# Optimization experiments

Hardware: AMD Instinct MI355X
Metric: run time of the kernel (lower is better)

## Reference

```python
import jax, jax.numpy as jnp
import numpy as np

DPITCH_RANGE = 24.0
SCALE = 1.0

B, T, ND, SD, H = 8192, 256, 8, 3, 64
HIST = 64
L = T - HIST  # generated LSTM steps; L+1 outputs emitted
IN = ND + SD + 1


def setup_inputs() -> dict:
    key = jax.random.key(0)
    ks = jax.random.split(key, 11)
    s = 1.0 / np.sqrt(H)

    def u(k, shape):
        return jax.random.uniform(k, shape, jnp.float32, -s, s)

    return {
        "noise": jax.random.normal(ks[0], (B, T, ND), jnp.float32),
        "hist_x": jax.random.normal(ks[1], (B, HIST, SD), jnp.float32) * 0.1,
        "gap_duration": jax.random.uniform(ks[2], (B, L + 1, SD - 1), jnp.float32),
        "W_ih": u(ks[3], (4 * H, IN)),
        "W_hh": u(ks[4], (4 * H, H)),
        "b_ih": u(ks[5], (4 * H,)),
        "b_hh": u(ks[6], (4 * H,)),
        "W1": u(ks[7], (H, H)),
        "b1": u(ks[8], (H,)),
        "W2": u(ks[9], (1, H)),
        "b2": u(ks[10], (1,)),
    }


def reference(noise, hist_x, gap_duration, W_ih, W_hh, b_ih, b_hh, W1, b1, W2, b2):
    hist_len = hist_x.shape[1]
    bias = b_ih + b_hh

    def lstm_cell(x, h, c):
        # PyTorch gate order: i, f, g, o
        gates = x @ W_ih.T + h @ W_hh.T + bias
        i, f, g, o = jnp.split(gates, 4, axis=-1)
        c = jax.nn.sigmoid(f) * c + jax.nn.sigmoid(i) * jnp.tanh(g)
        h = jax.nn.sigmoid(o) * jnp.tanh(c)
        return h, c

    # ---- conditioning on history ----
    dist = jnp.cumsum(hist_x[:, :, -1:], axis=1)                 # [B,HIST,1]
    cond_in = jnp.concatenate([hist_x, dist, noise[:, :hist_len]], axis=-1)  # [B,HIST,IN]
    h0 = jnp.zeros((noise.shape[0], W_hh.shape[1]), noise.dtype)
    c0 = jnp.zeros_like(h0)

    def cond_step(carry, x_t):
        h, c = carry
        h, c = lstm_cell(x_t, h, c)
        return (h, c), None

    (h, c), _ = jax.lax.scan(cond_step, (h0, c0), jnp.swapaxes(cond_in, 0, 1))
    output = h                      # last LSTM output [B,H]
    dist = dist[:, -1, :]           # [B,1]

    gen_noise = noise[:, hist_len:]                               # [B,L,ND]
    # pad one zero step: the final LSTM update is computed but unused
    gen_noise = jnp.concatenate(
        [gen_noise, jnp.zeros((gen_noise.shape[0], 1, gen_noise.shape[2]), gen_noise.dtype)], axis=1)
    xs = (jnp.swapaxes(gap_duration, 0, 1), jnp.swapaxes(gen_noise, 0, 1))

    def gen_step(carry, x_t):
        h, c, out, dist = carry
        gd, nz = x_t
        z = jnp.tanh(jnp.tanh(out @ W1.T + b1) @ W2.T + b2)       # output_net
        dp = z * DPITCH_RANGE * SCALE                             # [B,1]
        x = jnp.concatenate([gd, dp], axis=-1)                    # [B,SD]
        dist = dist + dp
        inp = jnp.concatenate([x, dist, nz], axis=-1)             # [B,IN]
        h, c = lstm_cell(inp, h, c)
        return (h, c, h, dist), x

    _, gen_xs = jax.lax.scan(gen_step, (h, c, output, dist), xs)  # [L+1,B,SD]
    output_seq = jnp.swapaxes(gen_xs, 0, 1)                       # [B,L+1,SD]
    return jnp.concatenate([hist_x, output_seq], axis=1)          # [B,HIST+L+1,SD]
```

## Files before the change

### kernel.cpp

```cpp
#include <hip/hip_runtime.h>
#include <stdint.h>

typedef unsigned short u16;
typedef unsigned int u32;
typedef __attribute__((ext_vector_type(8))) short short8v;
typedef __attribute__((ext_vector_type(4))) float f32x4;

#define NB 16
#define HISTN 64
#define TGEN 193

#define S_NOISE 2048
#define S_HIST  192
#define S_GAP   386
#define S_OUT   771

#define HROW 104

__device__ __forceinline__ float b2f(u16 u) { return __uint_as_float(((u32)u) << 16); }
__device__ __forceinline__ u16 f2b(float f) {
    u32 u = __float_as_uint(f);
    u32 r = (u + 0x7fffu + ((u >> 16) & 1u)) >> 16;
    return (u16)r;
}
__device__ __forceinline__ float rcp_(float x) { return __builtin_amdgcn_rcpf(x); }
__device__ __forceinline__ float sigf(float x) { return rcp_(1.0f + __expf(-x)); }
__device__ __forceinline__ float tanhf_(float x) {
    return __builtin_fmaf(-2.0f, rcp_(1.0f + __expf(2.0f * x)), 1.0f);
}
__device__ __forceinline__ float ldv(const void* p, int idx, bool f32) {
    return f32 ? ((const float*)p)[idx] : b2f(((const u16*)p)[idx]);
}
__device__ __forceinline__ void sync_lds() {
    asm volatile("s_waitcnt lgkmcnt(0)" ::: "memory");
    __builtin_amdgcn_s_barrier();
}

extern "C" __global__ void __launch_bounds__(512, 4)
lstm_gen_kernel(const void* __restrict__ noise, const void* __restrict__ hist_x,
                const void* __restrict__ gap, const void* __restrict__ pW_ih,
                const void* __restrict__ pW_hh, const void* __restrict__ pb_ih,
                const void* __restrict__ pb_hh, const void* __restrict__ pW1,
                const void* __restrict__ pb1, const void* __restrict__ pW2,
                const void* __restrict__ pb2, void* __restrict__ out)
{
    __shared__ u16 hst[NB * HROW];
    __shared__ float zpl[NB * 4];
    __shared__ float gds[TGEN][NB][2];
    __shared__ u16 nring[32][NB][8];
    __shared__ float dpd[NB];

    const int tid = threadIdx.x;
    const int lane = tid & 63;
    const int w = tid >> 6;
    const int lg = lane >> 4;
    const int ln = lane & 15;

    bool is_f32 = false;
    {
        const u32* p = (const u32*)pW_hh;
        for (int i = 0; i < 64; i++) {
            u32 v = p[i];
            float a = b2f((u16)(v & 0xffffu));
            float bb = b2f((u16)(v >> 16));
            if (!(fabsf(a) <= 0.5f) || !(fabsf(bb) <= 0.5f)) is_f32 = true;
        }
    }

    for (int i = tid; i < NB * HROW / 2; i += 512) ((u32*)hst)[i] = 0u;
    for (int i = tid; i < TGEN * NB * 2; i += 512) {
        int t = i >> 5, r = i & 31, b = r >> 1, k = r & 1;
        gds[t][b][k] = ldv(gap, ((size_t)blockIdx.x * NB + b) * S_GAP + t * 2 + k, is_f32);
    }

    short8v a00, a01, a02, a10, a11, a12;
#pragma unroll
    for (int T = 0; T < 2; T++) {
        const int j = (T << 5) | (w << 2) | (ln >> 2);
        const int g = ln & 3;
        const int row = (g << 6) | j;
        float wdp = ldv(pW_ih, row * 12 + 2, is_f32);
        u16 wdph = f2b(wdp);
        u16 wdpl = f2b(wdp - b2f(wdph));
        float wds = ldv(pW_ih, row * 12 + 3, is_f32);
        u16 wdsh = f2b(wds);
        u16 wdsl = f2b(wds - b2f(wdsh));
        short8v f0, f1, f2;
#pragma unroll
        for (int e = 0; e < 8; e++) {
            const int c = lg * 8 + e;
            f0[e] = (short)f2b(ldv(pW_hh, row * 64 + c, is_f32));
            f1[e] = (short)f2b(ldv(pW_hh, row * 64 + 32 + c, is_f32));
            u16 v = 0;
            if (c == 0 || c == 1) v = f2b(ldv(pW_ih, row * 12 + c, is_f32));
            else if (c == 2 || c == 3) v = wdph;
            else if (c == 4 || c == 5) v = wdsh;
            else if (c == 6) v = wdsl;
            else if (c == 7) v = wdpl;
            else if (c >= 8 && c < 16) v = f2b(ldv(pW_ih, row * 12 + (c - 4), is_f32));
            f2[e] = (short)v;
        }
        if (T == 0) { a00 = f0; a01 = f1; a02 = f2; }
        else        { a10 = f0; a11 = f1; a12 = f2; }
    }

    f32x4 bias0, bias1, wd0, wd1, ws0, ws1;
#pragma unroll
    for (int T = 0; T < 2; T++) {
        const int jc = (T << 5) | (w << 2) | lg;
        f32x4 bv, dv, sv;
#pragma unroll
        for (int q = 0; q < 4; q++) {
            const int row = (q << 6) | jc;
            bv[q] = ldv(pb_ih, row, is_f32) + ldv(pb_hh, row, is_f32);
            dv[q] = ldv(pW_ih, row * 12 + 2, is_f32);
            sv[q] = ldv(pW_ih, row * 12 + 3, is_f32);
        }
        if (T == 0) { bias0 = bv; wd0 = dv; ws0 = sv; }
        else        { bias1 = bv; wd1 = dv; ws1 = sv; }
    }

    const bool mlpw = (w >= 4);
    short8v w1F0 = {}, w1F1 = {};
    f32x4 b1v = {0.f, 0.f, 0.f, 0.f};
    float w2L[4] = {0.f, 0.f, 0.f, 0.f};
    if (mlpw) {
        const int wp = w - 4;
        const int row1 = (wp << 4) | ln;
#pragma unroll
        for (int e = 0; e < 8; e++) {
            w1F0[e] = (short)f2b(ldv(pW1, row1 * 64 + lg * 8 + e, is_f32));
            w1F1[e] = (short)f2b(ldv(pW1, row1 * 64 + 32 + lg * 8 + e, is_f32));
        }
        const int rq = (wp << 4) | (lg << 2);
#pragma unroll
        for (int q = 0; q < 4; q++) {
            b1v[q] = ldv(pb1, rq + q, is_f32);
            w2L[q] = ldv(pW2, rq + q, is_f32);
        }
    }

    const float b2v = ldv(pb2, 0, is_f32);

    const bool owner = tid < NB;
    const size_t gb = (size_t)blockIdx.x * NB + (size_t)(tid & (NB - 1));
    const u16* nz_h = (const u16*)noise + gb * S_NOISE;
    const float* nz_f = (const float*)noise + gb * S_NOISE;
    const u16* hx_h = (const u16*)hist_x + gb * S_HIST;
    const float* hx_f = (const float*)hist_x + gb * S_HIST;
    u16* out_h = (u16*)out + gb * S_OUT;
    float* out_f = (float*)out + gb * S_OUT;

    float dist = 0.0f;
    float cv0 = 0.f, cv1 = 0.f, cv2 = 0.f;
    u32 n01 = 0, n23 = 0, n45 = 0, n67 = 0;

    auto ldnoise = [&](int t) {
        if (is_f32) {
            const float4* q = (const float4*)(nz_f + t * 8);
            float4 a = q[0], bq = q[1];
            n01 = (u32)f2b(a.x) | ((u32)f2b(a.y) << 16);
            n23 = (u32)f2b(a.z) | ((u32)f2b(a.w) << 16);
            n45 = (u32)f2b(bq.x) | ((u32)f2b(bq.y) << 16);
            n67 = (u32)f2b(bq.z) | ((u32)f2b(bq.w) << 16);
        } else {
            uint4 nv = *(const uint4*)(nz_h + t * 8);
            n01 = nv.x; n23 = nv.y; n45 = nv.z; n67 = nv.w;
        }
    };

    if (owner) {
        if (is_f32) { cv0 = hx_f[0]; cv1 = hx_f[1]; cv2 = hx_f[2]; }
        else { cv0 = b2f(hx_h[0]); cv1 = b2f(hx_h[1]); cv2 = b2f(hx_h[2]); }
        ldnoise(0);
    }

    float cst0 = 0.f, cst1 = 0.f;
    __syncthreads();

#pragma unroll 1
    for (int t = 0; t < HISTN; t++) {
        short8v bf0 = *(const short8v*)&hst[ln * HROW + lg * 8];
        short8v bf1 = *(const short8v*)&hst[ln * HROW + 32 + lg * 8];
        if (owner) {
            dist += cv2;
            u16 dph = f2b(cv2); u16 dpl = f2b(cv2 - b2f(dph));
            u16 dsh = f2b(dist); u16 dsl = f2b(dist - b2f(dsh));
            u16* hr = &hst[tid * HROW];
            *(u32*)&hr[64] = (u32)f2b(cv0) | ((u32)f2b(cv1) << 16);
            *(u32*)&hr[66] = (u32)dph | ((u32)dpl << 16);
            *(u32*)&hr[68] = (u32)dsh | ((u32)dsl << 16);
            *(u32*)&hr[70] = (u32)dsh | ((u32)dph << 16);
            *(u32*)&hr[72] = n01; *(u32*)&hr[74] = n23;
            *(u32*)&hr[76] = n45; *(u32*)&hr[78] = n67;
        }
        sync_lds();
        if (owner) {
            if (is_f32) { out_f[t*3] = cv0; out_f[t*3+1] = cv1; out_f[t*3+2] = cv2; }
            else { out_h[t*3] = f2b(cv0); out_h[t*3+1] = f2b(cv1); out_h[t*3+2] = f2b(cv2); }
            if (t + 1 < HISTN) {
                if (is_f32) { cv0 = hx_f[(t+1)*3]; cv1 = hx_f[(t+1)*3+1]; cv2 = hx_f[(t+1)*3+2]; }
                else { cv0 = b2f(hx_h[(t+1)*3]); cv1 = b2f(hx_h[(t+1)*3+1]); cv2 = b2f(hx_h[(t+1)*3+2]); }
                ldnoise(t + 1);
            }
        }
        short8v bf2 = *(const short8v*)&hst[ln * HROW + 64 + lg * 8];
        f32x4 acc0 = bias0, acc1 = bias1;
        acc0 = __builtin_amdgcn_mfma_f32_16x16x32_bf16(a00, bf0, acc0, 0, 0, 0);
        acc0 = __builtin_amdgcn_mfma_f32_16x16x32_bf16(a01, bf1, acc0, 0, 0, 0);
        acc0 = __builtin_amdgcn_mfma_f32_16x16x32_bf16(a02, bf2, acc0, 0, 0, 0);
        acc1 = __builtin_amdgcn_mfma_f32_16x16x32_bf16(a10, bf0, acc1, 0, 0, 0);
        acc1 = __builtin_amdgcn_mfma_f32_16x16x32_bf16(a11, bf1, acc1, 0, 0, 0);
        acc1 = __builtin_amdgcn_mfma_f32_16x16x32_bf16(a12, bf2, acc1, 0, 0, 0);
        float h0, h1;
        { float iv = sigf(acc0[0]), fv = sigf(acc0[1]), gv = tanhf_(acc0[2]), ov = sigf(acc0[3]);
          cst0 = fv * cst0 + iv * gv; h0 = ov * tanhf_(cst0); }
        { float iv = sigf(acc1[0]), fv = sigf(acc1[1]), gv = tanhf_(acc1[2]), ov = sigf(acc1[3]);
          cst1 = fv * cst1 + iv * gv; h1 = ov * tanhf_(cst1); }
        const int j0 = (w << 2) | lg;
        hst[ln * HROW + j0] = f2b(h0);
        hst[ln * HROW + j0 + 32] = f2b(h1);
        sync_lds();
    }

    if (owner) dpd[tid] = dist;
    {
        const int s = tid >> 4, b = tid & 15;
        const int t = HISTN + s;
        u32 r0, r1, r2, r3;
        if (is_f32) {
            const float* nf = (const float*)noise + ((size_t)blockIdx.x * NB + b) * S_NOISE + t * 8;
            float4 a = *(const float4*)nf, bq = *(const float4*)(nf + 4);
            r0 = (u32)f2b(a.x) | ((u32)f2b(a.y) << 16);
            r1 = (u32)f2b(a.z) | ((u32)f2b(a.w) << 16);
            r2 = (u32)f2b(bq.x) | ((u32)f2b(bq.y) << 16);
            r3 = (u32)f2b(bq.z) | ((u32)f2b(bq.w) << 16);
        } else {
            uint4 nv = *(const uint4*)((const u16*)noise + ((size_t)blockIdx.x * NB + b) * S_NOISE + t * 8);
            r0 = nv.x; r1 = nv.y; r2 = nv.z; r3 = nv.w;
        }
        u32* dst = (u32*)&nring[s][b][0];
        dst[0] = r0; dst[1] = r1; dst[2] = r2; dst[3] = r3;
    }
    sync_lds();
    dist = dpd[ln];

#pragma unroll 1
    for (int tg = 0; tg < TGEN; tg++) {
        short8v bf0 = *(const short8v*)&hst[ln * HROW + lg * 8];
        short8v bf1 = *(const short8v*)&hst[ln * HROW + 32 + lg * 8];
        float2 g2 = *(const float2*)&gds[tg][ln][0];
        short8v bf2 = {};
        if (lg == 0) { bf2[0] = (short)f2b(g2.x); bf2[1] = (short)f2b(g2.y); }
        else if (lg == 1) {
            union { uint4 u; short8v s; } cvt;
            cvt.u = *(const uint4*)&nring[tg & 31][ln][0];
            bf2 = cvt.s;
        }
        f32x4 acc0 = bias0, acc1 = bias1;
        acc0 = __builtin_amdgcn_mfma_f32_16x16x32_bf16(a00, bf0, acc0, 0, 0, 0);
        acc0 = __builtin_amdgcn_mfma_f32_16x16x32_bf16(a01, bf1, acc0, 0, 0, 0);
        acc0 = __builtin_amdgcn_mfma_f32_16x16x32_bf16(a02, bf2, acc0, 0, 0, 0);
        acc1 = __builtin_amdgcn_mfma_f32_16x16x32_bf16(a10, bf0, acc1, 0, 0, 0);
        acc1 = __builtin_amdgcn_mfma_f32_16x16x32_bf16(a11, bf1, acc1, 0, 0, 0);
        acc1 = __builtin_amdgcn_mfma_f32_16x16x32_bf16(a12, bf2, acc1, 0, 0, 0);
        if (mlpw) {
            f32x4 m0 = b1v;
            m0 = __builtin_amdgcn_mfma_f32_16x16x32_bf16(w1F0, bf0, m0, 0, 0, 0);
            m0 = __builtin_amdgcn_mfma_f32_16x16x32_bf16(w1F1, bf1, m0, 0, 0, 0);
            float p = w2L[0] * tanhf_(m0[0]) + w2L[1] * tanhf_(m0[1])
                    + w2L[2] * tanhf_(m0[2]) + w2L[3] * tanhf_(m0[3]);
            p += __shfl_xor(p, 16);
            p += __shfl_xor(p, 32);
            if (lg == 0) zpl[(ln << 2) | (w - 4)] = p;
        }
        if (((tg & 15) == 0) && tg > 0 && tg <= 176 && tid < 256) {
            const int s = tid >> 4, b = tid & 15;
            const int t = HISTN + tg + 16 + s;
            u32 r0 = 0, r1 = 0, r2 = 0, r3 = 0;
            if (t < 256) {
                if (is_f32) {
                    const float* nf = (const float*)noise + ((size_t)blockIdx.x * NB + b) * S_NOISE + t * 8;
                    float4 a = *(const float4*)nf, bq = *(const float4*)(nf + 4);
                    r0 = (u32)f2b(a.x) | ((u32)f2b(a.y) << 16);
                    r1 = (u32)f2b(a.z) | ((u32)f2b(a.w) << 16);
                    r2 = (u32)f2b(bq.x) | ((u32)f2b(bq.y) << 16);
                    r3 = (u32)f2b(bq.z) | ((u32)f2b(bq.w) << 16);
                } else {
                    uint4 nv = *(const uint4*)((const u16*)noise + ((size_t)blockIdx.x * NB + b) * S_NOISE + t * 8);
                    r0 = nv.x; r1 = nv.y; r2 = nv.z; r3 = nv.w;
                }
            }
            u32* dst = (u32*)&nring[(tg + 16 + s) & 31][b][0];
            dst[0] = r0; dst[1] = r1; dst[2] = r2; dst[3] = r3;
        }
        sync_lds();
        f32x4 zr = *(const f32x4*)&zpl[ln << 2];
        float dp = 24.0f * tanhf_(b2v + zr[0] + zr[1] + zr[2] + zr[3]);
        dist += dp;
#pragma unroll
        for (int q = 0; q < 4; q++) {
            acc0[q] += wd0[q] * dp + ws0[q] * dist;
            acc1[q] += wd1[q] * dp + ws1[q] * dist;
        }
        float h0, h1;
        { float iv = sigf(acc0[0]), fv = sigf(acc0[1]), gv = tanhf_(acc0[2]), ov = sigf(acc0[3]);
          cst0 = fv * cst0 + iv * gv; h0 = ov * tanhf_(cst0); }
        { float iv = sigf(acc1[0]), fv = sigf(acc1[1]), gv = tanhf_(acc1[2]), ov = sigf(acc1[3]);
          cst1 = fv * cst1 + iv * gv; h1 = ov * tanhf_(cst1); }
        const int j0 = (w << 2) | lg;
        hst[ln * HROW + j0] = f2b(h0);
        hst[ln * HROW + j0 + 32] = f2b(h1);
        if (tid < NB) {
            const int to = HISTN + tg;
            if (is_f32) { out_f[to*3] = g2.x; out_f[to*3+1] = g2.y; out_f[to*3+2] = dp; }
            else { out_h[to*3] = f2b(g2.x); out_h[to*3+1] = f2b(g2.y); out_h[to*3+2] = f2b(dp); }
        }
        sync_lds();
    }
}

extern "C" void kernel_launch(void* const* d_in, const int* in_sizes, int n_in,
                              void* d_out, int out_size, void* d_ws, size_t ws_size,
                              hipStream_t stream) {
    (void)in_sizes; (void)n_in; (void)d_ws; (void)ws_size; (void)out_size;
    lstm_gen_kernel<<<512, 512, 0, stream>>>(
        d_in[0], d_in[1], d_in[2], d_in[3], d_in[4], d_in[5],
        d_in[6], d_in[7], d_in[8], d_in[9], d_in[10], d_out);
}
```

Baseline: 479.2 us.

## Fold log2e scaling into weights, precompute history inputs, double-buffer hidden state

Prescales the gate weights, biases and MLP weights by -log2(e) or 2·log2(e) so the activations can use the raw exp2 instruction instead of expf. The history-phase inputs (cumulative distance, noise) are precomputed into LDS before the loop, and the hist_x copy to the output moves out of the serial recurrence. The history loop double-buffers the hidden state, which removes one barrier per step. Gap values are stored in LDS as packed bf16, and the hidden outputs are packed with v_cvt_pk_bf16_f32. Rounding the prescaled weights to bf16 slightly changes numerics and the added LDS arrays increase shared memory use.

```diff
diff --git a/kernel.cpp b/kernel.cpp
--- a/kernel.cpp
+++ b/kernel.cpp
@@ -16,6 +16,8 @@
 #define S_OUT   771
 
 #define HROW 104
+#define L2E  1.442695041f
+#define L2E2 2.885390082f
 
 __device__ __forceinline__ float b2f(u16 u) { return __uint_as_float(((u32)u) << 16); }
 __device__ __forceinline__ u16 f2b(float f) {
@@ -24,9 +26,20 @@
     return (u16)r;
 }
 __device__ __forceinline__ float rcp_(float x) { return __builtin_amdgcn_rcpf(x); }
-__device__ __forceinline__ float sigf(float x) { return rcp_(1.0f + __expf(-x)); }
-__device__ __forceinline__ float tanhf_(float x) {
-    return __builtin_fmaf(-2.0f, rcp_(1.0f + __expf(2.0f * x)), 1.0f);
+__device__ __forceinline__ float ex2(float x) { return __builtin_amdgcn_exp2f(x); }
+__device__ __forceinline__ u32 cvtpk(float a, float b) {
+    u32 r; asm("v_cvt_pk_bf16_f32 %0, %1, %2" : "=v"(r) : "v"(a), "v"(b)); return r;
+}
+__device__ __forceinline__ float tanh2(float s) {
+    return __builtin_fmaf(-2.0f, rcp_(1.0f + ex2(s)), 1.0f);
+}
+__device__ __forceinline__ float cellh(const f32x4 a, float& c) {
+    float iv = rcp_(1.0f + ex2(a[0]));
+    float fv = rcp_(1.0f + ex2(a[1]));
+    float gv = tanh2(a[2]);
+    float ov = rcp_(1.0f + ex2(a[3]));
+    c = __builtin_fmaf(fv, c, iv * gv);
+    return ov * tanh2(L2E2 * c);
 }
 __device__ __forceinline__ float ldv(const void* p, int idx, bool f32) {
     return f32 ? ((const float*)p)[idx] : b2f(((const u16*)p)[idx]);
@@ -44,10 +57,12 @@
                 const void* __restrict__ pb1, const void* __restrict__ pW2,
                 const void* __restrict__ pb2, void* __restrict__ out)
 {
-    __shared__ u16 hst[NB * HROW];
+    __shared__ u16 hb[2][NB * HROW];
+    __shared__ u16 cxsA[HISTN][NB][8];
+    __shared__ u16 cxsB[HISTN][NB][8];
+    __shared__ u32 gdsb[TGEN * NB];
+    __shared__ u16 nring[32][NB][8];
     __shared__ float zpl[NB * 4];
-    __shared__ float gds[TGEN][NB][2];
-    __shared__ u16 nring[32][NB][8];
     __shared__ float dpd[NB];
 
     const int tid = threadIdx.x;
@@ -67,10 +82,78 @@
         }
     }
 
-    for (int i = tid; i < NB * HROW / 2; i += 512) ((u32*)hst)[i] = 0u;
-    for (int i = tid; i < TGEN * NB * 2; i += 512) {
-        int t = i >> 5, r = i & 31, b = r >> 1, k = r & 1;
-        gds[t][b][k] = ldv(gap, ((size_t)blockIdx.x * NB + b) * S_GAP + t * 2 + k, is_f32);
+    float* hs = (float*)gdsb;
+
+    for (int i = tid; i < NB * HROW; i += 512) ((u32*)hb)[i] = 0u;
+    for (int i = tid; i < HISTN * NB * 3; i += 512) {
+        int t = i / 48, r = i % 48, b = r / 3, k = r % 3;
+        hs[i] = ldv(hist_x, ((size_t)blockIdx.x * NB + b) * S_HIST + t * 3 + k, is_f32);
+    }
+    for (int i = tid; i < HISTN * NB * 4; i += 512) {
+        int t = i >> 6, r = i & 63, b = r >> 2, q = r & 3;
+        size_t base = ((size_t)blockIdx.x * NB + b) * S_NOISE + t * 8;
+        u32 v;
+        if (is_f32) {
+            const float* p = (const float*)noise + base + q * 2;
+            v = (u32)f2b(p[0]) | ((u32)f2b(p[1]) << 16);
+        } else v = ((const u32*)noise)[(base >> 1) + q];
+        ((u32*)&cxsB[t][b][0])[q] = v;
+    }
+    {
+        const int s = tid >> 4, b = tid & 15;
+        size_t base = ((size_t)blockIdx.x * NB + b) * S_NOISE + (size_t)(HISTN + s) * 8;
+        u32 r0, r1, r2, r3;
+        if (is_f32) {
+            const float* nf = (const float*)noise + base;
+            float4 a = *(const float4*)nf, bq = *(const float4*)(nf + 4);
+            r0 = (u32)f2b(a.x) | ((u32)f2b(a.y) << 16);
+            r1 = (u32)f2b(a.z) | ((u32)f2b(a.w) << 16);
+            r2 = (u32)f2b(bq.x) | ((u32)f2b(bq.y) << 16);
+            r3 = (u32)f2b(bq.z) | ((u32)f2b(bq.w) << 16);
+        } else {
+            uint4 nv = *(const uint4*)((const u16*)noise + base);
+            r0 = nv.x; r1 = nv.y; r2 = nv.z; r3 = nv.w;
+        }
+        u32* dst = (u32*)&nring[s][b][0];
+        dst[0] = r0; dst[1] = r1; dst[2] = r2; dst[3] = r3;
+    }
+    for (int i = tid; i < NB * HISTN * 3; i += 512) {
+        int b = i / 192, e = i % 192;
+        size_t bt = (size_t)blockIdx.x * NB + b;
+        if (is_f32) ((float*)out)[bt * S_OUT + e] = ((const float*)hist_x)[bt * S_HIST + e];
+        else ((u16*)out)[bt * S_OUT + e] = ((const u16*)hist_x)[bt * S_HIST + e];
+    }
+    __syncthreads();
+
+    if (tid < NB) {
+        float dd = 0.0f;
+#pragma unroll 1
+        for (int t = 0; t < HISTN; t++) {
+            float x0 = hs[t * 48 + tid * 3 + 0];
+            float x1 = hs[t * 48 + tid * 3 + 1];
+            float x2 = hs[t * 48 + tid * 3 + 2];
+            dd += x2;
+            u16 dph = f2b(x2); u16 dpl = f2b(x2 - b2f(dph));
+            u16 dsh = f2b(dd); u16 dsl = f2b(dd - b2f(dsh));
+            u32* dst = (u32*)&cxsA[t][tid][0];
+            dst[0] = (u32)f2b(x0) | ((u32)f2b(x1) << 16);
+            dst[1] = (u32)dph | ((u32)dpl << 16);
+            dst[2] = (u32)dsh | ((u32)dsl << 16);
+            dst[3] = (u32)dsh | ((u32)dph << 16);
+        }
+        dpd[tid] = dd;
+    }
+    __syncthreads();
+
+    for (int i = tid; i < TGEN * NB; i += 512) {
+        int t = i >> 4, b = i & 15;
+        size_t base = ((size_t)blockIdx.x * NB + b) * S_GAP + t * 2;
+        u32 v;
+        if (is_f32) {
+            const float* p = (const float*)gap + base;
+            v = (u32)f2b(p[0]) | ((u32)f2b(p[1]) << 16);
+        } else v = *(const u32*)((const u16*)gap + base);
+        gdsb[i] = v;
     }
 
     short8v a00, a01, a02, a10, a11, a12;
@@ -79,25 +162,24 @@
         const int j = (T << 5) | (w << 2) | (ln >> 2);
         const int g = ln & 3;
         const int row = (g << 6) | j;
-        float wdp = ldv(pW_ih, row * 12 + 2, is_f32);
-        u16 wdph = f2b(wdp);
-        u16 wdpl = f2b(wdp - b2f(wdph));
-        float wds = ldv(pW_ih, row * 12 + 3, is_f32);
-        u16 wdsh = f2b(wds);
-        u16 wdsl = f2b(wds - b2f(wdsh));
+        const float rs = (g == 2) ? L2E2 : -L2E;
+        float wdp = ldv(pW_ih, row * 12 + 2, is_f32) * rs;
+        u16 wdph = f2b(wdp); u16 wdpl = f2b(wdp - b2f(wdph));
+        float wds = ldv(pW_ih, row * 12 + 3, is_f32) * rs;
+        u16 wdsh = f2b(wds); u16 wdsl = f2b(wds - b2f(wdsh));
         short8v f0, f1, f2;
 #pragma unroll
         for (int e = 0; e < 8; e++) {
             const int c = lg * 8 + e;
-            f0[e] = (short)f2b(ldv(pW_hh, row * 64 + c, is_f32));
-            f1[e] = (short)f2b(ldv(pW_hh, row * 64 + 32 + c, is_f32));
+            f0[e] = (short)f2b(ldv(pW_hh, row * 64 + c, is_f32) * rs);
+            f1[e] = (short)f2b(ldv(pW_hh, row * 64 + 32 + c, is_f32) * rs);
             u16 v = 0;
-            if (c == 0 || c == 1) v = f2b(ldv(pW_ih, row * 12 + c, is_f32));
+            if (c == 0 || c == 1) v = f2b(ldv(pW_ih, row * 12 + c, is_f32) * rs);
             else if (c == 2 || c == 3) v = wdph;
             else if (c == 4 || c == 5) v = wdsh;
             else if (c == 6) v = wdsl;
             else if (c == 7) v = wdpl;
-            else if (c >= 8 && c < 16) v = f2b(ldv(pW_ih, row * 12 + (c - 4), is_f32));
+            else if (c >= 8 && c < 16) v = f2b(ldv(pW_ih, row * 12 + (c - 4), is_f32) * rs);
             f2[e] = (short)v;
         }
         if (T == 0) { a00 = f0; a01 = f1; a02 = f2; }
@@ -112,9 +194,10 @@
 #pragma unroll
         for (int q = 0; q < 4; q++) {
             const int row = (q << 6) | jc;
-            bv[q] = ldv(pb_ih, row, is_f32) + ldv(pb_hh, row, is_f32);
-            dv[q] = ldv(pW_ih, row * 12 + 2, is_f32);
-            sv[q] = ldv(pW_ih, row * 12 + 3, is_f32);
+            const float qs = (q == 2) ? L2E2 : -L2E;
+            bv[q] = (ldv(pb_ih, row, is_f32) + ldv(pb_hh, row, is_f32)) * qs;
+            dv[q] = ldv(pW_ih, row * 12 + 2, is_f32) * qs;
+            sv[q] = ldv(pW_ih, row * 12 + 3, is_f32) * qs;
         }
         if (T == 0) { bias0 = bv; wd0 = dv; ws0 = sv; }
         else        { bias1 = bv; wd1 = dv; ws1 = sv; }
@@ -129,82 +212,36 @@
         const int row1 = (wp << 4) | ln;
 #pragma unroll
         for (int e = 0; e < 8; e++) {
-            w1F0[e] = (short)f2b(ldv(pW1, row1 * 64 + lg * 8 + e, is_f32));
-            w1F1[e] = (short)f2b(ldv(pW1, row1 * 64 + 32 + lg * 8 + e, is_f32));
+            w1F0[e] = (short)f2b(ldv(pW1, row1 * 64 + lg * 8 + e, is_f32) * L2E2);
+            w1F1[e] = (short)f2b(ldv(pW1, row1 * 64 + 32 + lg * 8 + e, is_f32) * L2E2);
         }
         const int rq = (wp << 4) | (lg << 2);
 #pragma unroll
         for (int q = 0; q < 4; q++) {
-            b1v[q] = ldv(pb1, rq + q, is_f32);
-            w2L[q] = ldv(pW2, rq + q, is_f32);
-        }
-    }
-
-    const float b2v = ldv(pb2, 0, is_f32);
-
-    const bool owner = tid < NB;
-    const size_t gb = (size_t)blockIdx.x * NB + (size_t)(tid & (NB - 1));
-    const u16* nz_h = (const u16*)noise + gb * S_NOISE;
-    const float* nz_f = (const float*)noise + gb * S_NOISE;
-    const u16* hx_h = (const u16*)hist_x + gb * S_HIST;
-    const float* hx_f = (const float*)hist_x + gb * S_HIST;
+            b1v[q] = ldv(pb1, rq + q, is_f32) * L2E2;
+            w2L[q] = ldv(pW2, rq + q, is_f32) * L2E2;
+        }
+    }
+    const float b2vs = ldv(pb2, 0, is_f32) * L2E2;
+
+    const size_t gb = (size_t)blockIdx.x * NB + (size_t)ln;
+    const float* gd_f = (const float*)gap + gb * S_GAP;
     u16* out_h = (u16*)out + gb * S_OUT;
     float* out_f = (float*)out + gb * S_OUT;
 
-    float dist = 0.0f;
-    float cv0 = 0.f, cv1 = 0.f, cv2 = 0.f;
-    u32 n01 = 0, n23 = 0, n45 = 0, n67 = 0;
-
-    auto ldnoise = [&](int t) {
-        if (is_f32) {
-            const float4* q = (const float4*)(nz_f + t * 8);
-            float4 a = q[0], bq = q[1];
-            n01 = (u32)f2b(a.x) | ((u32)f2b(a.y) << 16);
-            n23 = (u32)f2b(a.z) | ((u32)f2b(a.w) << 16);
-            n45 = (u32)f2b(bq.x) | ((u32)f2b(bq.y) << 16);
-            n67 = (u32)f2b(bq.z) | ((u32)f2b(bq.w) << 16);
-        } else {
-            uint4 nv = *(const uint4*)(nz_h + t * 8);
-            n01 = nv.x; n23 = nv.y; n45 = nv.z; n67 = nv.w;
-        }
-    };
-
-    if (owner) {
-        if (is_f32) { cv0 = hx_f[0]; cv1 = hx_f[1]; cv2 = hx_f[2]; }
-        else { cv0 = b2f(hx_h[0]); cv1 = b2f(hx_h[1]); cv2 = b2f(hx_h[2]); }
-        ldnoise(0);
-    }
-
     float cst0 = 0.f, cst1 = 0.f;
+    int pc = 0;
     __syncthreads();
 
 #pragma unroll 1
     for (int t = 0; t < HISTN; t++) {
-        short8v bf0 = *(const short8v*)&hst[ln * HROW + lg * 8];
-        short8v bf1 = *(const short8v*)&hst[ln * HROW + 32 + lg * 8];
-        if (owner) {
-            dist += cv2;
-            u16 dph = f2b(cv2); u16 dpl = f2b(cv2 - b2f(dph));
-            u16 dsh = f2b(dist); u16 dsl = f2b(dist - b2f(dsh));
-            u16* hr = &hst[tid * HROW];
-            *(u32*)&hr[64] = (u32)f2b(cv0) | ((u32)f2b(cv1) << 16);
-            *(u32*)&hr[66] = (u32)dph | ((u32)dpl << 16);
-            *(u32*)&hr[68] = (u32)dsh | ((u32)dsl << 16);
-            *(u32*)&hr[70] = (u32)dsh | ((u32)dph << 16);
-            *(u32*)&hr[72] = n01; *(u32*)&hr[74] = n23;
-            *(u32*)&hr[76] = n45; *(u32*)&hr[78] = n67;
-        }
-        sync_lds();
-        if (owner) {
-            if (is_f32) { out_f[t*3] = cv0; out_f[t*3+1] = cv1; out_f[t*3+2] = cv2; }
-            else { out_h[t*3] = f2b(cv0); out_h[t*3+1] = f2b(cv1); out_h[t*3+2] = f2b(cv2); }
-            if (t + 1 < HISTN) {
-                if (is_f32) { cv0 = hx_f[(t+1)*3]; cv1 = hx_f[(t+1)*3+1]; cv2 = hx_f[(t+1)*3+2]; }
-                else { cv0 = b2f(hx_h[(t+1)*3]); cv1 = b2f(hx_h[(t+1)*3+1]); cv2 = b2f(hx_h[(t+1)*3+2]); }
-                ldnoise(t + 1);
-            }
-        }
-        short8v bf2 = *(const short8v*)&hst[ln * HROW + 64 + lg * 8];
+        const u16* hc = hb[pc];
+        u16* hn = hb[pc ^ 1];
+        short8v bf0 = *(const short8v*)&hc[ln * HROW + lg * 8];
+        short8v bf1 = *(const short8v*)&hc[ln * HROW + 32 + lg * 8];
+        short8v bf2 = {};
+        if (lg == 0) bf2 = *(const short8v*)&cxsA[t][ln][0];
+        else if (lg == 1) bf2 = *(const short8v*)&cxsB[t][ln][0];
         f32x4 acc0 = bias0, acc1 = bias1;
         acc0 = __builtin_amdgcn_mfma_f32_16x16x32_bf16(a00, bf0, acc0, 0, 0, 0);
         acc0 = __builtin_amdgcn_mfma_f32_16x16x32_bf16(a01, bf1, acc0, 0, 0, 0);
@@ -212,47 +249,31 @@
         acc1 = __builtin_amdgcn_mfma_f32_16x16x32_bf16(a10, bf0, acc1, 0, 0, 0);
         acc1 = __builtin_amdgcn_mfma_f32_16x16x32_bf16(a11, bf1, acc1, 0, 0, 0);
         acc1 = __builtin_amdgcn_mfma_f32_16x16x32_bf16(a12, bf2, acc1, 0, 0, 0);
-        float h0, h1;
-        { float iv = sigf(acc0[0]), fv = sigf(acc0[1]), gv = tanhf_(acc0[2]), ov = sigf(acc0[3]);
-          cst0 = fv * cst0 + iv * gv; h0 = ov * tanhf_(cst0); }
-        { float iv = sigf(acc1[0]), fv = sigf(acc1[1]), gv = tanhf_(acc1[2]), ov = sigf(acc1[3]);
-          cst1 = fv * cst1 + iv * gv; h1 = ov * tanhf_(cst1); }
+        float h0 = cellh(acc0, cst0);
+        float h1 = cellh(acc1, cst1);
+        u32 hp = cvtpk(h0, h1);
         const int j0 = (w << 2) | lg;
-        hst[ln * HROW + j0] = f2b(h0);
-        hst[ln * HROW + j0 + 32] = f2b(h1);
+        hn[ln * HROW + j0] = (u16)hp;
+        hn[ln * HROW + j0 + 32] = (u16)(hp >> 16);
         sync_lds();
-    }
-
-    if (owner) dpd[tid] = dist;
-    {
-        const int s = tid >> 4, b = tid & 15;
-        const int t = HISTN + s;
-        u32 r0, r1, r2, r3;
-        if (is_f32) {
-            const float* nf = (const float*)noise + ((size_t)blockIdx.x * NB + b) * S_NOISE + t * 8;
-            float4 a = *(const float4*)nf, bq = *(const float4*)(nf + 4);
-            r0 = (u32)f2b(a.x) | ((u32)f2b(a.y) << 16);
-            r1 = (u32)f2b(a.z) | ((u32)f2b(a.w) << 16);
-            r2 = (u32)f2b(bq.x) | ((u32)f2b(bq.y) << 16);
-            r3 = (u32)f2b(bq.z) | ((u32)f2b(bq.w) << 16);
-        } else {
-            uint4 nv = *(const uint4*)((const u16*)noise + ((size_t)blockIdx.x * NB + b) * S_NOISE + t * 8);
-            r0 = nv.x; r1 = nv.y; r2 = nv.z; r3 = nv.w;
-        }
-        u32* dst = (u32*)&nring[s][b][0];
-        dst[0] = r0; dst[1] = r1; dst[2] = r2; dst[3] = r3;
-    }
-    sync_lds();
-    dist = dpd[ln];
+        pc ^= 1;
+    }
+
+    float dist = dpd[ln];
+    float gdf0 = 0.f, gdf1 = 0.f;
+    if (is_f32 && tid < NB) { gdf0 = gd_f[0]; gdf1 = gd_f[1]; }
 
 #pragma unroll 1
     for (int tg = 0; tg < TGEN; tg++) {
-        short8v bf0 = *(const short8v*)&hst[ln * HROW + lg * 8];
-        short8v bf1 = *(const short8v*)&hst[ln * HROW + 32 + lg * 8];
-        float2 g2 = *(const float2*)&gds[tg][ln][0];
+        u16* hB = hb[0];
+        short8v bf0 = *(const short8v*)&hB[ln * HROW + lg * 8];
+        short8v bf1 = *(const short8v*)&hB[ln * HROW + 32 + lg * 8];
         short8v bf2 = {};
-        if (lg == 0) { bf2[0] = (short)f2b(g2.x); bf2[1] = (short)f2b(g2.y); }
-        else if (lg == 1) {
+        u32 g32 = 0;
+        if (lg == 0) {
+            g32 = gdsb[(tg << 4) | ln];
+            bf2[0] = (short)(g32 & 0xffffu); bf2[1] = (short)(g32 >> 16);
+        } else if (lg == 1) {
             union { uint4 u; short8v s; } cvt;
             cvt.u = *(const uint4*)&nring[tg & 31][ln][0];
             bf2 = cvt.s;
@@ -268,26 +289,27 @@
             f32x4 m0 = b1v;
             m0 = __builtin_amdgcn_mfma_f32_16x16x32_bf16(w1F0, bf0, m0, 0, 0, 0);
             m0 = __builtin_amdgcn_mfma_f32_16x16x32_bf16(w1F1, bf1, m0, 0, 0, 0);
-            float p = w2L[0] * tanhf_(m0[0]) + w2L[1] * tanhf_(m0[1])
-                    + w2L[2] * tanhf_(m0[2]) + w2L[3] * tanhf_(m0[3]);
-            p += __shfl_xor(p, 16);
-            p += __shfl_xor(p, 32);
-            if (lg == 0) zpl[(ln << 2) | (w - 4)] = p;
+            float mp = w2L[0] * tanh2(m0[0]) + w2L[1] * tanh2(m0[1])
+                     + w2L[2] * tanh2(m0[2]) + w2L[3] * tanh2(m0[3]);
+            mp += __shfl_xor(mp, 16);
+            mp += __shfl_xor(mp, 32);
+            if (lg == 0) zpl[(ln << 2) | (w - 4)] = mp;
         }
         if (((tg & 15) == 0) && tg > 0 && tg <= 176 && tid < 256) {
             const int s = tid >> 4, b = tid & 15;
             const int t = HISTN + tg + 16 + s;
             u32 r0 = 0, r1 = 0, r2 = 0, r3 = 0;
             if (t < 256) {
+                size_t base = ((size_t)blockIdx.x * NB + b) * S_NOISE + (size_t)t * 8;
                 if (is_f32) {
-                    const float* nf = (const float*)noise + ((size_t)blockIdx.x * NB + b) * S_NOISE + t * 8;
+                    const float* nf = (const float*)noise + base;
                     float4 a = *(const float4*)nf, bq = *(const float4*)(nf + 4);
                     r0 = (u32)f2b(a.x) | ((u32)f2b(a.y) << 16);
                     r1 = (u32)f2b(a.z) | ((u32)f2b(a.w) << 16);
                     r2 = (u32)f2b(bq.x) | ((u32)f2b(bq.y) << 16);
                     r3 = (u32)f2b(bq.z) | ((u32)f2b(bq.w) << 16);
                 } else {
-                    uint4 nv = *(const uint4*)((const u16*)noise + ((size_t)blockIdx.x * NB + b) * S_NOISE + t * 8);
+                    uint4 nv = *(const uint4*)((const u16*)noise + base);
                     r0 = nv.x; r1 = nv.y; r2 = nv.z; r3 = nv.w;
                 }
             }
@@ -296,25 +318,30 @@
         }
         sync_lds();
         f32x4 zr = *(const f32x4*)&zpl[ln << 2];
-        float dp = 24.0f * tanhf_(b2v + zr[0] + zr[1] + zr[2] + zr[3]);
+        float th = tanh2(b2vs + zr[0] + zr[1] + zr[2] + zr[3]);
+        float dp = 24.0f * th;
         dist += dp;
 #pragma unroll
         for (int q = 0; q < 4; q++) {
             acc0[q] += wd0[q] * dp + ws0[q] * dist;
             acc1[q] += wd1[q] * dp + ws1[q] * dist;
         }
-        float h0, h1;
-        { float iv = sigf(acc0[0]), fv = sigf(acc0[1]), gv = tanhf_(acc0[2]), ov = sigf(acc0[3]);
-          cst0 = fv * cst0 + iv * gv; h0 = ov * tanhf_(cst0); }
-        { float iv = sigf(acc1[0]), fv = sigf(acc1[1]), gv = tanhf_(acc1[2]), ov = sigf(acc1[3]);
-          cst1 = fv * cst1 + iv * gv; h1 = ov * tanhf_(cst1); }
+        float h0 = cellh(acc0, cst0);
+        float h1 = cellh(acc1, cst1);
+        u32 hp = cvtpk(h0, h1);
         const int j0 = (w << 2) | lg;
-        hst[ln * HROW + j0] = f2b(h0);
-        hst[ln * HROW + j0 + 32] = f2b(h1);
+        hB[ln * HROW + j0] = (u16)hp;
+        hB[ln * HROW + j0 + 32] = (u16)(hp >> 16);
         if (tid < NB) {
             const int to = HISTN + tg;
-            if (is_f32) { out_f[to*3] = g2.x; out_f[to*3+1] = g2.y; out_f[to*3+2] = dp; }
-            else { out_h[to*3] = f2b(g2.x); out_h[to*3+1] = f2b(g2.y); out_h[to*3+2] = f2b(dp); }
+            if (is_f32) {
+                out_f[to * 3] = gdf0; out_f[to * 3 + 1] = gdf1; out_f[to * 3 + 2] = dp;
+                if (tg + 1 < TGEN) { gdf0 = gd_f[(tg + 1) * 2]; gdf1 = gd_f[(tg + 1) * 2 + 1]; }
+            } else {
+                out_h[to * 3] = (u16)(g32 & 0xffffu);
+                out_h[to * 3 + 1] = (u16)(g32 >> 16);
+                out_h[to * 3 + 2] = f2b(dp);
+            }
         }
         sync_lds();
     }
```

After: 435.8 us. 1.1x faster.
